# Kernel optimization log

Hardware: AMD Instinct MI355X
Metric: run time of the kernel (lower is better)

The kernel has to match this reference:

```python
import jax, jax.numpy as jnp
import numpy as np

DIM = 1024
HEADS = 16
HEAD_DIM = DIM // HEADS
FEAT = 256
B, N = 4, 4096


def setup_inputs() -> dict:
    key = jax.random.key(0)
    ks = jax.random.split(key, 10)
    s = 1.0 / np.sqrt(DIM)
    return {
        "x": jax.random.normal(ks[0], (B, N, DIM), jnp.float32),
        "Wq": jax.random.normal(ks[1], (DIM, DIM), jnp.float32) * s,
        "bq": jnp.zeros((DIM,), jnp.float32),
        "Wk": jax.random.normal(ks[2], (DIM, DIM), jnp.float32) * s,
        "bk": jnp.zeros((DIM,), jnp.float32),
        "Wv": jax.random.normal(ks[3], (DIM, DIM), jnp.float32) * s,
        "bv": jnp.zeros((DIM,), jnp.float32),
        "Wo": jax.random.normal(ks[4], (DIM, DIM), jnp.float32) * s,
        "bo": jnp.zeros((DIM,), jnp.float32),
        "random_features": jax.random.normal(ks[5], (HEAD_DIM, FEAT), jnp.float32) / np.sqrt(FEAT),
    }


def reference(x, Wq, bq, Wk, bk, Wv, bv, Wo, bo, random_features):
    Bsz, Nlen, C = x.shape
    # linear projections, reshape to (B, N, H, head_dim)
    q = (x @ Wq + bq).reshape(Bsz, Nlen, HEADS, HEAD_DIM)
    k = (x @ Wk + bk).reshape(Bsz, Nlen, HEADS, HEAD_DIM)
    v = (x @ Wv + bv).reshape(Bsz, Nlen, HEADS, HEAD_DIM)
    # positive feature map: elu(x)+1
    q = jax.nn.elu(q) + 1.0
    k = jax.nn.elu(k) + 1.0
    # random-feature projection (B, N, H, F)
    q = jnp.einsum('bnhd,df->bnhf', q, random_features)
    k = jnp.einsum('bnhd,df->bnhf', k, random_features)
    # kernelized linear attention (no normalization, non-causal as in source)
    kv = jnp.einsum('bnhf,bnhd->bhfd', k, v)          # (B, H, F, head_dim)
    out = jnp.einsum('bnhf,bhfd->bnhd', q, kv)        # (B, N, H, head_dim)
    out = out.reshape(Bsz, Nlen, C)
    return out @ Wo + bo
```

## Files before the change

### kernel.cpp

```cpp
#include <hip/hip_runtime.h>
#include <hip/hip_bf16.h>
#include <cstdint>
#include <cstddef>

using bf16 = __hip_bfloat16;
typedef __attribute__((ext_vector_type(8))) __bf16 bf16x8;
typedef __attribute__((ext_vector_type(4))) float f32x4;

typedef const __attribute__((address_space(1))) void CGV;
typedef __attribute__((address_space(3))) void LDSV;

__device__ __forceinline__ void gload_lds16(const void* g, void* l) {
    __builtin_amdgcn_global_load_lds((CGV*)g, (LDSV*)l, 16, 0, 0);
}

__device__ __forceinline__ float bits2f(unsigned short u) {
    return __uint_as_float(((unsigned)u) << 16);
}
__device__ __forceinline__ unsigned short f2bits(float f) {
    return __builtin_bit_cast(unsigned short, __float2bfloat16(f));
}

__global__ __launch_bounds__(256) void prep_kernel(
    const float4* __restrict__ x4, ushort4* __restrict__ Xb4,
    const float* __restrict__ Wq, const float* __restrict__ Wk,
    const float* __restrict__ Wv, bf16* __restrict__ Wt3,
    const float* __restrict__ RF, float* __restrict__ G)
{
    const int bi = blockIdx.x;
    const int t = threadIdx.x;
    if (bi < 16384) {
        int i = bi * 256 + t;
        float4 f = x4[i];
        ushort4 u;
        u.x = f2bits(f.x); u.y = f2bits(f.y); u.z = f2bits(f.z); u.w = f2bits(f.w);
        Xb4[i] = u;
    } else if (bi < 19456) {
        int rem = bi - 16384;
        int z = rem >> 10;
        int r2 = rem & 1023;
        int bx = r2 & 31, by = r2 >> 5;
        const float* W = (z == 0) ? Wq : (z == 1) ? Wk : Wv;
        bf16* O = Wt3 + (size_t)z * (1024 * 1024);
        __shared__ float tile[32][33];
        int tx = t & 31, ty = t >> 5;
        int xg = bx * 32 + tx;
        int y0 = by * 32;
        for (int i = ty; i < 32; i += 8)
            tile[i][tx] = W[(size_t)(y0 + i) * 1024 + xg];
        __syncthreads();
        int xo = by * 32 + tx;
        int yo = bx * 32;
        for (int i = ty; i < 32; i += 8)
            O[(size_t)(yo + i) * 1024 + xo] = __float2bfloat16(tile[tx][i]);
    } else {
        int o = (bi - 19456) * 256 + t;
        int i = o >> 6, j = o & 63;
        const float4* a = (const float4*)(RF + (size_t)i * 256);
        const float4* b = (const float4*)(RF + (size_t)j * 256);
        float s = 0.f;
        for (int f = 0; f < 64; f++) {
            float4 xx = a[f], yy = b[f];
            s += xx.x * yy.x + xx.y * yy.y + xx.z * yy.z + xx.w * yy.w;
        }
        G[o] = s;
    }
}

__global__ __launch_bounds__(256, 4) void gemm_qkv(
    const bf16* __restrict__ X, const bf16* __restrict__ Wt3,
    const float* __restrict__ bq, const float* __restrict__ bk, const float* __restrict__ bv,
    bf16* __restrict__ Qo, bf16* __restrict__ Ko, bf16* __restrict__ Vo)
{
    __shared__ bf16 As[128 * 64];
    __shared__ bf16 Bs[128 * 64];
    const int z = blockIdx.z;
    const int lid = blockIdx.x + (blockIdx.y << 3);
    const int xcd = lid & 7, seq = lid >> 3;
    const int m0 = (xcd * 16 + (seq >> 3)) * 128;
    const int n0 = (seq & 7) * 128;
    const int tid = threadIdx.x;
    const int w = tid >> 6, lane = tid & 63;
    const int lr = lane >> 3, lc = lane & 7;
    const int sc = lc ^ lr;
    const bf16* Wt = Wt3 + (size_t)z * (1024 * 1024);

    const bf16* ag = X  + (size_t)(m0 + w * 32 + lr) * 1024 + sc * 8;
    const bf16* bg = Wt + (size_t)(n0 + w * 32 + lr) * 1024 + sc * 8;
    bf16* al = As + (w * 32) * 64;
    bf16* bl = Bs + (w * 32) * 64;

    f32x4 acc[4][4];
#pragma unroll
    for (int i = 0; i < 4; i++)
#pragma unroll
        for (int j = 0; j < 4; j++) acc[i][j] = (f32x4){0.f, 0.f, 0.f, 0.f};

    const int lm = lane & 15, quad = lane >> 4;
    const int x0 = (quad ^ (lm & 7)) * 8;
    const int x1 = ((quad + 4) ^ (lm & 7)) * 8;
    const bf16* Ab = As + ((w >> 1) * 64 + lm) * 64;
    const bf16* Bb = Bs + ((w & 1) * 64 + lm) * 64;

    for (int k0 = 0; k0 < 1024; k0 += 64) {
#pragma unroll
        for (int j = 0; j < 4; j++) {
            gload_lds16(ag + (size_t)j * 8 * 1024 + k0, al + j * 8 * 64);
            gload_lds16(bg + (size_t)j * 8 * 1024 + k0, bl + j * 8 * 64);
        }
        __syncthreads();
#pragma unroll
        for (int kk = 0; kk < 2; kk++) {
            const int xo = kk ? x1 : x0;
            bf16x8 a[4], b[4];
#pragma unroll
            for (int i = 0; i < 4; i++) a[i] = *(const bf16x8*)(Ab + i * 16 * 64 + xo);
#pragma unroll
            for (int i = 0; i < 4; i++) b[i] = *(const bf16x8*)(Bb + i * 16 * 64 + xo);
#pragma unroll
            for (int mi = 0; mi < 4; mi++)
#pragma unroll
                for (int ni = 0; ni < 4; ni++)
                    acc[mi][ni] = __builtin_amdgcn_mfma_f32_16x16x32_bf16(
                        a[mi], b[ni], acc[mi][ni], 0, 0, 0);
        }
        __syncthreads();
    }

    const int wr = (w >> 1) * 64, wc = (w & 1) * 64;
    if (z == 0) {
#pragma unroll
        for (int ni = 0; ni < 4; ni++) {
            int col = n0 + wc + ni * 16 + lm;
            float bs = bq[col];
#pragma unroll
            for (int mi = 0; mi < 4; mi++) {
                int row0 = m0 + wr + mi * 16 + quad * 4;
#pragma unroll
                for (int r = 0; r < 4; r++) {
                    float v = acc[mi][ni][r] + bs;
                    v = (v > 0.f) ? (v + 1.f) : __expf(v);
                    Qo[(size_t)(row0 + r) * 1024 + col] = __float2bfloat16(v);
                }
            }
        }
    } else {
        const float* bias = (z == 1) ? bk : bv;
        bf16* Out = (z == 1) ? Ko : Vo;
#pragma unroll
        for (int ni = 0; ni < 4; ni++) {
            int col = n0 + wc + ni * 16 + lm;
            float bs = bias[col];
            int h = col >> 6, d = col & 63;
#pragma unroll
            for (int mi = 0; mi < 4; mi++) {
                int row0 = m0 + wr + mi * 16 + quad * 4;
#pragma unroll
                for (int r = 0; r < 4; r++) {
                    int row = row0 + r;
                    int b = row >> 12, n = row & 4095;
                    float v = acc[mi][ni][r] + bs;
                    if (z == 1) v = (v > 0.f) ? (v + 1.f) : __expf(v);
                    Out[(((size_t)(b * 16 + h) * 4096 + n) << 6) + d] = __float2bfloat16(v);
                }
            }
        }
    }
}

__global__ __launch_bounds__(256, 2) void s_kernel(const bf16* __restrict__ Kp,
                                                   const bf16* __restrict__ Vp,
                                                   float* __restrict__ Spart)
{
    __shared__ bf16 Ks[256 * 64];
    __shared__ bf16 Vs[256 * 64];
    const int bh = blockIdx.x, sp = blockIdx.y;
    const int t = threadIdx.x;
    const int w = t >> 6, lane = t & 63;
    const int eb = (t >> 4) * 4, db = (t & 15) * 4;
    const size_t base = ((size_t)bh * 4096 + sp * 512) * 64;

    float acc[4][4];
#pragma unroll
    for (int i = 0; i < 4; i++)
#pragma unroll
        for (int j = 0; j < 4; j++) acc[i][j] = 0.f;

    const unsigned short* ks = (const unsigned short*)Ks;
    const unsigned short* vs = (const unsigned short*)Vs;

    for (int tile = 0; tile < 2; tile++) {
        const bf16* kg = Kp + base + tile * (256 * 64) + (size_t)w * 4096 + lane * 8;
        const bf16* vg = Vp + base + tile * (256 * 64) + (size_t)w * 4096 + lane * 8;
#pragma unroll
        for (int r = 0; r < 8; r++) {
            gload_lds16(kg + r * 512, Ks + w * 4096 + r * 512);
            gload_lds16(vg + r * 512, Vs + w * 4096 + r * 512);
        }
        __syncthreads();
#pragma unroll 4
        for (int n = 0; n < 256; n++) {
            ushort4 ku = *(const ushort4*)(ks + n * 64 + eb);
            ushort4 vu = *(const ushort4*)(vs + n * 64 + db);
            float kf[4] = {bits2f(ku.x), bits2f(ku.y), bits2f(ku.z), bits2f(ku.w)};
            float vf[4] = {bits2f(vu.x), bits2f(vu.y), bits2f(vu.z), bits2f(vu.w)};
#pragma unroll
            for (int i = 0; i < 4; i++)
#pragma unroll
                for (int j = 0; j < 4; j++) acc[i][j] += kf[i] * vf[j];
        }
        __syncthreads();
    }

    float* spb = Spart + ((size_t)sp * 64 + bh) * 4096;
#pragma unroll
    for (int i = 0; i < 4; i++)
#pragma unroll
        for (int j = 0; j < 4; j++) spb[(eb + i) * 64 + db + j] = acc[i][j];
}

__global__ __launch_bounds__(256) void fold2_kernel(const float* __restrict__ Spart,
                                                    const float* __restrict__ G,
                                                    const float* __restrict__ Wo,
                                                    bf16* __restrict__ Wo2t)
{
    __shared__ float Sl[4096];
    __shared__ float Ml[4096];
    const int xb = blockIdx.x;
    const int b = xb >> 6, h = (xb >> 2) & 15, cb = xb & 3;
    const int bh = b * 16 + h;
    const int t = threadIdx.x;

    for (int i = t; i < 4096; i += 256) {
        float s = 0.f;
#pragma unroll
        for (int sp = 0; sp < 8; sp++)
            s += Spart[((size_t)sp * 64 + bh) * 4096 + i];
        Sl[i] = s;
    }
    __syncthreads();

    {
        const int e = t >> 2, dblk = (t & 3) * 16;
        float acc[16];
#pragma unroll
        for (int j = 0; j < 16; j++) acc[j] = 0.f;
        for (int ep = 0; ep < 64; ep++) {
            float g = G[e * 64 + ep];
#pragma unroll
            for (int j = 0; j < 16; j++) acc[j] += g * Sl[ep * 64 + dblk + j];
        }
        __syncthreads();
#pragma unroll
        for (int j = 0; j < 16; j++) Ml[(dblk + j) * 64 + e] = acc[j];
    }
    __syncthreads();

    const int c = cb * 256 + t;
    float acc[64];
#pragma unroll
    for (int e = 0; e < 64; e++) acc[e] = 0.f;
    for (int d = 0; d < 64; d++) {
        float wo = Wo[(size_t)(h * 64 + d) * 1024 + c];
#pragma unroll
        for (int e = 0; e < 64; e++) acc[e] += Ml[d * 64 + e] * wo;
    }
    unsigned* outp = (unsigned*)(Wo2t + ((size_t)b * 1024 + c) * 1024 + h * 64);
#pragma unroll
    for (int e = 0; e < 64; e += 2) {
        unsigned lo = f2bits(acc[e]);
        unsigned hi = f2bits(acc[e + 1]);
        outp[e >> 1] = lo | (hi << 16);
    }
}

__global__ __launch_bounds__(256, 4) void gemm_out(
    const bf16* __restrict__ Qp, const bf16* __restrict__ Wo2t,
    const float* __restrict__ bo, float* __restrict__ Out)
{
    __shared__ bf16 As[128 * 64];
    __shared__ bf16 Bs[128 * 64];
    const int lid = blockIdx.x + (blockIdx.y << 3);
    const int xcd = lid & 7, seq = lid >> 3;
    const int m0 = (xcd * 16 + (seq >> 3)) * 128;
    const int n0 = (seq & 7) * 128;
    const int tid = threadIdx.x;
    const int w = tid >> 6, lane = tid & 63;
    const int lr = lane >> 3, lc = lane & 7;
    const int sc = lc ^ lr;
    const bf16* Wt = Wo2t + (size_t)(m0 >> 12) * (1024 * 1024);

    const bf16* ag = Qp + (size_t)(m0 + w * 32 + lr) * 1024 + sc * 8;
    const bf16* bg = Wt + (size_t)(n0 + w * 32 + lr) * 1024 + sc * 8;
    bf16* al = As + (w * 32) * 64;
    bf16* bl = Bs + (w * 32) * 64;

    f32x4 acc[4][4];
#pragma unroll
    for (int i = 0; i < 4; i++)
#pragma unroll
        for (int j = 0; j < 4; j++) acc[i][j] = (f32x4){0.f, 0.f, 0.f, 0.f};

    const int lm = lane & 15, quad = lane >> 4;
    const int x0 = (quad ^ (lm & 7)) * 8;
    const int x1 = ((quad + 4) ^ (lm & 7)) * 8;
    const bf16* Ab = As + ((w >> 1) * 64 + lm) * 64;
    const bf16* Bb = Bs + ((w & 1) * 64 + lm) * 64;

    for (int k0 = 0; k0 < 1024; k0 += 64) {
#pragma unroll
        for (int j = 0; j < 4; j++) {
            gload_lds16(ag + (size_t)j * 8 * 1024 + k0, al + j * 8 * 64);
            gload_lds16(bg + (size_t)j * 8 * 1024 + k0, bl + j * 8 * 64);
        }
        __syncthreads();
#pragma unroll
        for (int kk = 0; kk < 2; kk++) {
            const int xo = kk ? x1 : x0;
            bf16x8 a[4], b[4];
#pragma unroll
            for (int i = 0; i < 4; i++) a[i] = *(const bf16x8*)(Ab + i * 16 * 64 + xo);
#pragma unroll
            for (int i = 0; i < 4; i++) b[i] = *(const bf16x8*)(Bb + i * 16 * 64 + xo);
#pragma unroll
            for (int mi = 0; mi < 4; mi++)
#pragma unroll
                for (int ni = 0; ni < 4; ni++)
                    acc[mi][ni] = __builtin_amdgcn_mfma_f32_16x16x32_bf16(
                        a[mi], b[ni], acc[mi][ni], 0, 0, 0);
        }
        __syncthreads();
    }

    const int wr = (w >> 1) * 64, wc = (w & 1) * 64;
#pragma unroll
    for (int ni = 0; ni < 4; ni++) {
        int col = n0 + wc + ni * 16 + lm;
        float bs = bo[col];
#pragma unroll
        for (int mi = 0; mi < 4; mi++) {
            int row0 = m0 + wr + mi * 16 + quad * 4;
#pragma unroll
            for (int r = 0; r < 4; r++)
                Out[(size_t)(row0 + r) * 1024 + col] = acc[mi][ni][r] + bs;
        }
    }
}

extern "C" void kernel_launch(void* const* d_in, const int* in_sizes, int n_in,
                              void* d_out, int out_size, void* d_ws, size_t ws_size,
                              hipStream_t stream) {
    const float* x  = (const float*)d_in[0];
    const float* Wq = (const float*)d_in[1];
    const float* bq = (const float*)d_in[2];
    const float* Wk = (const float*)d_in[3];
    const float* bk = (const float*)d_in[4];
    const float* Wv = (const float*)d_in[5];
    const float* bv = (const float*)d_in[6];
    const float* Wo = (const float*)d_in[7];
    const float* bo = (const float*)d_in[8];
    const float* RF = (const float*)d_in[9];
    float* out = (float*)d_out;

    char* ws = (char*)d_ws;
    bf16*  Xb    = (bf16*) (ws);
    bf16*  Qp    = (bf16*) (ws + ((size_t)32  << 20));
    bf16*  Kp    = (bf16*) (ws + ((size_t)64  << 20));
    bf16*  Vp    = (bf16*) (ws + ((size_t)96  << 20));
    bf16*  Wt3   = (bf16*) (ws + ((size_t)128 << 20));
    bf16*  Wo2t  = (bf16*) (ws + ((size_t)134 << 20));
    float* Spart = (float*)(ws + ((size_t)142 << 20));
    float* G     = (float*)(ws + ((size_t)152 << 20));

    prep_kernel<<<19472, 256, 0, stream>>>((const float4*)x, (ushort4*)Xb,
                                           Wq, Wk, Wv, Wt3, RF, G);
    gemm_qkv<<<dim3(8, 128, 3), 256, 0, stream>>>(Xb, Wt3, bq, bk, bv, Qp, Kp, Vp);
    s_kernel<<<dim3(64, 8), 256, 0, stream>>>(Kp, Vp, Spart);
    fold2_kernel<<<256, 256, 0, stream>>>(Spart, G, Wo, Wo2t);
    gemm_out<<<dim3(8, 128), 256, 0, stream>>>(Qp, Wo2t, bo, out);
}
```

Measured before the change: 379.8 us.

## Fuse K/V projection with per-tile K^T V reduction, drop K/V materialization

Splits the QKV GEMM into a Q-only GEMM and a fused K/V GEMM that shares the X tile between both weight matrices and computes the per-128-row K^T V partial product in its epilogue using MFMA through LDS. The per-tile partial products are written to a partial buffer and summed by a new reduce kernel, and the fold kernel now reads the reduced S directly. This removes the 32 MB bf16 writes and rereads of K and V and the scalar-FMA s_kernel. In exchange there are more partial sums (32 per head instead of 8), the fused kernel needs twice the accumulator registers, which costs occupancy, and launch bounds are lowered to 2 waves per SIMD.

```diff
diff --git a/kernel.cpp b/kernel.cpp
--- a/kernel.cpp
+++ b/kernel.cpp
@@ -67,14 +67,12 @@
     }
 }
 
-__global__ __launch_bounds__(256, 4) void gemm_qkv(
+__global__ __launch_bounds__(256, 2) void gemm_q(
     const bf16* __restrict__ X, const bf16* __restrict__ Wt3,
-    const float* __restrict__ bq, const float* __restrict__ bk, const float* __restrict__ bv,
-    bf16* __restrict__ Qo, bf16* __restrict__ Ko, bf16* __restrict__ Vo)
+    const float* __restrict__ bq, bf16* __restrict__ Qo)
 {
     __shared__ bf16 As[128 * 64];
     __shared__ bf16 Bs[128 * 64];
-    const int z = blockIdx.z;
     const int lid = blockIdx.x + (blockIdx.y << 3);
     const int xcd = lid & 7, seq = lid >> 3;
     const int m0 = (xcd * 16 + (seq >> 3)) * 128;
@@ -83,10 +81,9 @@
     const int w = tid >> 6, lane = tid & 63;
     const int lr = lane >> 3, lc = lane & 7;
     const int sc = lc ^ lr;
-    const bf16* Wt = Wt3 + (size_t)z * (1024 * 1024);
-
-    const bf16* ag = X  + (size_t)(m0 + w * 32 + lr) * 1024 + sc * 8;
-    const bf16* bg = Wt + (size_t)(n0 + w * 32 + lr) * 1024 + sc * 8;
+
+    const bf16* ag = X   + (size_t)(m0 + w * 32 + lr) * 1024 + sc * 8;
+    const bf16* bg = Wt3 + (size_t)(n0 + w * 32 + lr) * 1024 + sc * 8;
     bf16* al = As + (w * 32) * 64;
     bf16* bl = Bs + (w * 32) * 64;
 
@@ -128,98 +125,173 @@
     }
 
     const int wr = (w >> 1) * 64, wc = (w & 1) * 64;
-    if (z == 0) {
-#pragma unroll
-        for (int ni = 0; ni < 4; ni++) {
-            int col = n0 + wc + ni * 16 + lm;
-            float bs = bq[col];
-#pragma unroll
-            for (int mi = 0; mi < 4; mi++) {
-                int row0 = m0 + wr + mi * 16 + quad * 4;
-#pragma unroll
-                for (int r = 0; r < 4; r++) {
-                    float v = acc[mi][ni][r] + bs;
-                    v = (v > 0.f) ? (v + 1.f) : __expf(v);
-                    Qo[(size_t)(row0 + r) * 1024 + col] = __float2bfloat16(v);
+#pragma unroll
+    for (int ni = 0; ni < 4; ni++) {
+        int col = n0 + wc + ni * 16 + lm;
+        float bs = bq[col];
+#pragma unroll
+        for (int mi = 0; mi < 4; mi++) {
+            int row0 = m0 + wr + mi * 16 + quad * 4;
+#pragma unroll
+            for (int r = 0; r < 4; r++) {
+                float v = acc[mi][ni][r] + bs;
+                v = (v > 0.f) ? (v + 1.f) : __expf(v);
+                Qo[(size_t)(row0 + r) * 1024 + col] = __float2bfloat16(v);
+            }
+        }
+    }
+}
+
+__global__ __launch_bounds__(256, 2) void gemm_kvs(
+    const bf16* __restrict__ X, const bf16* __restrict__ Wt3,
+    const float* __restrict__ bk, const float* __restrict__ bv,
+    float* __restrict__ Spart2)
+{
+    __shared__ bf16 smem[24576];
+    bf16* As  = smem;
+    bf16* Bks = smem + 8192;
+    bf16* Bvs = smem + 16384;
+
+    const int lid = blockIdx.x + (blockIdx.y << 3);
+    const int xcd = lid & 7, seq = lid >> 3;
+    const int m0 = (xcd * 16 + (seq >> 3)) * 128;
+    const int n0 = (seq & 7) * 128;
+    const int tid = threadIdx.x;
+    const int w = tid >> 6, lane = tid & 63;
+    const int lr = lane >> 3, lc = lane & 7;
+    const int sc = lc ^ lr;
+
+    const bf16* ag  = X + (size_t)(m0 + w * 32 + lr) * 1024 + sc * 8;
+    const bf16* bgk = Wt3 + (size_t)(1 << 20) + (size_t)(n0 + w * 32 + lr) * 1024 + sc * 8;
+    const bf16* bgv = Wt3 + (size_t)(2 << 20) + (size_t)(n0 + w * 32 + lr) * 1024 + sc * 8;
+    bf16* al  = As  + (w * 32) * 64;
+    bf16* blk = Bks + (w * 32) * 64;
+    bf16* blv = Bvs + (w * 32) * 64;
+
+    f32x4 acck[4][4], accv[4][4];
+#pragma unroll
+    for (int i = 0; i < 4; i++)
+#pragma unroll
+        for (int j = 0; j < 4; j++) {
+            acck[i][j] = (f32x4){0.f, 0.f, 0.f, 0.f};
+            accv[i][j] = (f32x4){0.f, 0.f, 0.f, 0.f};
+        }
+
+    const int lm = lane & 15, quad = lane >> 4;
+    const int x0 = (quad ^ (lm & 7)) * 8;
+    const int x1 = ((quad + 4) ^ (lm & 7)) * 8;
+    const bf16* Ab  = As  + ((w >> 1) * 64 + lm) * 64;
+    const bf16* Bbk = Bks + ((w & 1) * 64 + lm) * 64;
+    const bf16* Bbv = Bvs + ((w & 1) * 64 + lm) * 64;
+
+    for (int k0 = 0; k0 < 1024; k0 += 64) {
+#pragma unroll
+        for (int j = 0; j < 4; j++) {
+            gload_lds16(ag  + (size_t)j * 8 * 1024 + k0, al  + j * 8 * 64);
+            gload_lds16(bgk + (size_t)j * 8 * 1024 + k0, blk + j * 8 * 64);
+            gload_lds16(bgv + (size_t)j * 8 * 1024 + k0, blv + j * 8 * 64);
+        }
+        __syncthreads();
+#pragma unroll
+        for (int kk = 0; kk < 2; kk++) {
+            const int xo = kk ? x1 : x0;
+            bf16x8 a[4], bb[4];
+#pragma unroll
+            for (int i = 0; i < 4; i++) a[i] = *(const bf16x8*)(Ab + i * 16 * 64 + xo);
+#pragma unroll
+            for (int i = 0; i < 4; i++) bb[i] = *(const bf16x8*)(Bbk + i * 16 * 64 + xo);
+#pragma unroll
+            for (int mi = 0; mi < 4; mi++)
+#pragma unroll
+                for (int ni = 0; ni < 4; ni++)
+                    acck[mi][ni] = __builtin_amdgcn_mfma_f32_16x16x32_bf16(
+                        a[mi], bb[ni], acck[mi][ni], 0, 0, 0);
+#pragma unroll
+            for (int i = 0; i < 4; i++) bb[i] = *(const bf16x8*)(Bbv + i * 16 * 64 + xo);
+#pragma unroll
+            for (int mi = 0; mi < 4; mi++)
+#pragma unroll
+                for (int ni = 0; ni < 4; ni++)
+                    accv[mi][ni] = __builtin_amdgcn_mfma_f32_16x16x32_bf16(
+                        a[mi], bb[ni], accv[mi][ni], 0, 0, 0);
+        }
+        __syncthreads();
+    }
+
+    const int b = m0 >> 12, mt = (m0 & 4095) >> 7;
+    const int h0 = n0 >> 6;
+    const int wr = (w >> 1) * 64;
+    const int myh = w & 1;
+
+#pragma unroll
+    for (int ih = 0; ih < 2; ih++) {
+        __syncthreads();
+        if (myh == ih) {
+#pragma unroll
+            for (int ni = 0; ni < 4; ni++) {
+                int lc2 = ni * 16 + lm;
+                int col = n0 + myh * 64 + lc2;
+                float bsk = bk[col], bsv = bv[col];
+#pragma unroll
+                for (int mi = 0; mi < 4; mi++) {
+                    int row = wr + mi * 16 + quad * 4;
+                    ushort4 kp, vp;
+                    {
+                        float v0 = acck[mi][ni][0] + bsk; v0 = (v0 > 0.f) ? (v0 + 1.f) : __expf(v0);
+                        float v1 = acck[mi][ni][1] + bsk; v1 = (v1 > 0.f) ? (v1 + 1.f) : __expf(v1);
+                        float v2 = acck[mi][ni][2] + bsk; v2 = (v2 > 0.f) ? (v2 + 1.f) : __expf(v2);
+                        float v3 = acck[mi][ni][3] + bsk; v3 = (v3 > 0.f) ? (v3 + 1.f) : __expf(v3);
+                        kp.x = f2bits(v0); kp.y = f2bits(v1); kp.z = f2bits(v2); kp.w = f2bits(v3);
+                    }
+                    {
+                        float v0 = accv[mi][ni][0] + bsv;
+                        float v1 = accv[mi][ni][1] + bsv;
+                        float v2 = accv[mi][ni][2] + bsv;
+                        float v3 = accv[mi][ni][3] + bsv;
+                        vp.x = f2bits(v0); vp.y = f2bits(v1); vp.z = f2bits(v2); vp.w = f2bits(v3);
+                    }
+                    *(ushort4*)&smem[lc2 * 136 + row]        = kp;
+                    *(ushort4*)&smem[8704 + lc2 * 136 + row] = vp;
                 }
             }
         }
-    } else {
-        const float* bias = (z == 1) ? bk : bv;
-        bf16* Out = (z == 1) ? Ko : Vo;
-#pragma unroll
-        for (int ni = 0; ni < 4; ni++) {
-            int col = n0 + wc + ni * 16 + lm;
-            float bs = bias[col];
-            int h = col >> 6, d = col & 63;
-#pragma unroll
-            for (int mi = 0; mi < 4; mi++) {
-                int row0 = m0 + wr + mi * 16 + quad * 4;
-#pragma unroll
-                for (int r = 0; r < 4; r++) {
-                    int row = row0 + r;
-                    int b = row >> 12, n = row & 4095;
-                    float v = acc[mi][ni][r] + bs;
-                    if (z == 1) v = (v > 0.f) ? (v + 1.f) : __expf(v);
-                    Out[(((size_t)(b * 16 + h) * 4096 + n) << 6) + d] = __float2bfloat16(v);
-                }
+        __syncthreads();
+        f32x4 sacc[4];
+#pragma unroll
+        for (int dt = 0; dt < 4; dt++) sacc[dt] = (f32x4){0.f, 0.f, 0.f, 0.f};
+#pragma unroll
+        for (int ks = 0; ks < 4; ks++) {
+            bf16x8 af = *(const bf16x8*)&smem[(w * 16 + lm) * 136 + ks * 32 + quad * 8];
+#pragma unroll
+            for (int dt = 0; dt < 4; dt++) {
+                bf16x8 bf = *(const bf16x8*)&smem[8704 + (dt * 16 + lm) * 136 + ks * 32 + quad * 8];
+                sacc[dt] = __builtin_amdgcn_mfma_f32_16x16x32_bf16(af, bf, sacc[dt], 0, 0, 0);
             }
         }
-    }
-}
-
-__global__ __launch_bounds__(256, 2) void s_kernel(const bf16* __restrict__ Kp,
-                                                   const bf16* __restrict__ Vp,
-                                                   float* __restrict__ Spart)
-{
-    __shared__ bf16 Ks[256 * 64];
-    __shared__ bf16 Vs[256 * 64];
-    const int bh = blockIdx.x, sp = blockIdx.y;
-    const int t = threadIdx.x;
-    const int w = t >> 6, lane = t & 63;
-    const int eb = (t >> 4) * 4, db = (t & 15) * 4;
-    const size_t base = ((size_t)bh * 4096 + sp * 512) * 64;
-
-    float acc[4][4];
-#pragma unroll
-    for (int i = 0; i < 4; i++)
-#pragma unroll
-        for (int j = 0; j < 4; j++) acc[i][j] = 0.f;
-
-    const unsigned short* ks = (const unsigned short*)Ks;
-    const unsigned short* vs = (const unsigned short*)Vs;
-
-    for (int tile = 0; tile < 2; tile++) {
-        const bf16* kg = Kp + base + tile * (256 * 64) + (size_t)w * 4096 + lane * 8;
-        const bf16* vg = Vp + base + tile * (256 * 64) + (size_t)w * 4096 + lane * 8;
-#pragma unroll
-        for (int r = 0; r < 8; r++) {
-            gload_lds16(kg + r * 512, Ks + w * 4096 + r * 512);
-            gload_lds16(vg + r * 512, Vs + w * 4096 + r * 512);
-        }
-        __syncthreads();
-#pragma unroll 4
-        for (int n = 0; n < 256; n++) {
-            ushort4 ku = *(const ushort4*)(ks + n * 64 + eb);
-            ushort4 vu = *(const ushort4*)(vs + n * 64 + db);
-            float kf[4] = {bits2f(ku.x), bits2f(ku.y), bits2f(ku.z), bits2f(ku.w)};
-            float vf[4] = {bits2f(vu.x), bits2f(vu.y), bits2f(vu.z), bits2f(vu.w)};
-#pragma unroll
-            for (int i = 0; i < 4; i++)
-#pragma unroll
-                for (int j = 0; j < 4; j++) acc[i][j] += kf[i] * vf[j];
-        }
-        __syncthreads();
-    }
-
-    float* spb = Spart + ((size_t)sp * 64 + bh) * 4096;
-#pragma unroll
-    for (int i = 0; i < 4; i++)
-#pragma unroll
-        for (int j = 0; j < 4; j++) spb[(eb + i) * 64 + db + j] = acc[i][j];
-}
-
-__global__ __launch_bounds__(256) void fold2_kernel(const float* __restrict__ Spart,
+        float* sb = Spart2 + (((size_t)(b * 16 + h0 + ih) * 32 + mt) << 12);
+#pragma unroll
+        for (int dt = 0; dt < 4; dt++)
+#pragma unroll
+            for (int r = 0; r < 4; r++)
+                sb[(w * 16 + quad * 4 + r) * 64 + dt * 16 + lm] = sacc[dt][r];
+    }
+}
+
+__global__ __launch_bounds__(256) void reduce_s2(const float* __restrict__ Spart2,
+                                                 float* __restrict__ S)
+{
+    const int bh = blockIdx.x, t = threadIdx.x;
+    const float* base = Spart2 + ((size_t)bh << 17);
+    for (int j = 0; j < 16; j++) {
+        int i = j * 256 + t;
+        float s = 0.f;
+#pragma unroll
+        for (int mtl = 0; mtl < 32; mtl++) s += base[(mtl << 12) + i];
+        S[((size_t)bh << 12) + i] = s;
+    }
+}
+
+__global__ __launch_bounds__(256) void fold2_kernel(const float* __restrict__ S,
                                                     const float* __restrict__ G,
                                                     const float* __restrict__ Wo,
                                                     bf16* __restrict__ Wo2t)
@@ -231,13 +303,7 @@
     const int bh = b * 16 + h;
     const int t = threadIdx.x;
 
-    for (int i = t; i < 4096; i += 256) {
-        float s = 0.f;
-#pragma unroll
-        for (int sp = 0; sp < 8; sp++)
-            s += Spart[((size_t)sp * 64 + bh) * 4096 + i];
-        Sl[i] = s;
-    }
+    for (int i = t; i < 4096; i += 256) Sl[i] = S[((size_t)bh << 12) + i];
     __syncthreads();
 
     {
@@ -274,7 +340,7 @@
     }
 }
 
-__global__ __launch_bounds__(256, 4) void gemm_out(
+__global__ __launch_bounds__(256, 2) void gemm_out(
     const bf16* __restrict__ Qp, const bf16* __restrict__ Wo2t,
     const float* __restrict__ bo, float* __restrict__ Out)
 {
@@ -363,19 +429,19 @@
     float* out = (float*)d_out;
 
     char* ws = (char*)d_ws;
-    bf16*  Xb    = (bf16*) (ws);
-    bf16*  Qp    = (bf16*) (ws + ((size_t)32  << 20));
-    bf16*  Kp    = (bf16*) (ws + ((size_t)64  << 20));
-    bf16*  Vp    = (bf16*) (ws + ((size_t)96  << 20));
-    bf16*  Wt3   = (bf16*) (ws + ((size_t)128 << 20));
-    bf16*  Wo2t  = (bf16*) (ws + ((size_t)134 << 20));
-    float* Spart = (float*)(ws + ((size_t)142 << 20));
-    float* G     = (float*)(ws + ((size_t)152 << 20));
+    bf16*  Xb     = (bf16*) (ws);
+    bf16*  Qp     = (bf16*) (ws + ((size_t)32  << 20));
+    bf16*  Wt3    = (bf16*) (ws + ((size_t)64  << 20));
+    bf16*  Wo2t   = (bf16*) (ws + ((size_t)70  << 20));
+    float* Spart2 = (float*)(ws + ((size_t)80  << 20));
+    float* S      = (float*)(ws + ((size_t)112 << 20));
+    float* G      = (float*)(ws + ((size_t)113 << 20));
 
     prep_kernel<<<19472, 256, 0, stream>>>((const float4*)x, (ushort4*)Xb,
                                            Wq, Wk, Wv, Wt3, RF, G);
-    gemm_qkv<<<dim3(8, 128, 3), 256, 0, stream>>>(Xb, Wt3, bq, bk, bv, Qp, Kp, Vp);
-    s_kernel<<<dim3(64, 8), 256, 0, stream>>>(Kp, Vp, Spart);
-    fold2_kernel<<<256, 256, 0, stream>>>(Spart, G, Wo, Wo2t);
+    gemm_q<<<dim3(8, 128), 256, 0, stream>>>(Xb, Wt3, bq, Qp);
+    gemm_kvs<<<dim3(8, 128), 256, 0, stream>>>(Xb, Wt3, bk, bv, Spart2);
+    reduce_s2<<<64, 256, 0, stream>>>(Spart2, S);
+    fold2_kernel<<<256, 256, 0, stream>>>(S, G, Wo, Wo2t);
     gemm_out<<<dim3(8, 128), 256, 0, stream>>>(Qp, Wo2t, bo, out);
 }
```

New measurement: 400.1 us. 1.05x slower.
